# Kernel optimization log

Hardware: AMD Instinct MI355X
Metric: run time of the kernel (lower is better)

Reference implementation:

```python
import jax, jax.numpy as jnp
import numpy as np
from jax import lax

RADIUS = [1, 3, 5, 9, 13, 21]
RATE = 1
K = 4            # shift radius -> (2K+1)^2 = 81 shifts
EPS = 1e-8       # torch.cosine_similarity eps


def setup_inputs() -> dict:
    key = jax.random.key(0)
    k1, k2, k3, k4 = jax.random.split(key, 4)
    b, cin, cout, h, w = 2, 128, 128, 96, 128
    x = jax.random.normal(k1, (b, cout, h, w), dtype=jnp.float32)
    y = jax.random.normal(k2, (b, cin, h, w), dtype=jnp.float32)
    # 6 dilated conv branches, all Conv2d(cin, cout, 3) -> stacked (6, O, I, 3, 3)
    weights = jax.random.normal(k3, (6, cout, cin, 3, 3), dtype=jnp.float32) * 0.05
    biases = jax.random.normal(k4, (6, cout), dtype=jnp.float32) * 0.05
    return {"x": x, "y": y, "weights": weights, "biases": biases}


def _forward(x, y, weights, biases):
    b, c, h, w = y.shape
    k = K
    # reflect-pad y by k, then 'same' dilated convs (zero padding = dilation)
    y_pad = jnp.pad(y, ((0, 0), (0, 0), (k, k), (k, k)), mode="reflect")

    # precompute grouped query features and their norms once
    xg = x.reshape(b, 4, -1, h, w)                      # (b,4,c/4,h,w)
    xn = jnp.sqrt(jnp.sum(xg * xg, axis=2))             # (b,4,h,w)

    # per-branch conv outputs over the padded extent, grouped, with cached norms
    branches = []
    for idx, r in enumerate(RADIUS):
        d = r * RATE
        yo = lax.conv_general_dilated(
            y_pad, weights[idx], window_strides=(1, 1),
            padding=[(d, d), (d, d)], rhs_dilation=(d, d),
            dimension_numbers=("NCHW", "OIHW", "NCHW"),
        ) + biases[idx][None, :, None, None]            # (b,cout,h+2k,w+2k)
        yg = yo.reshape(b, 4, -1, h + 2 * k, w + 2 * k)
        yn = jnp.sqrt(jnp.sum(yg * yg, axis=2))          # (b,4,h+2k,w+2k)
        branches.append((yg, yn))

    result = []
    for i in range(-k, k + 1):
        for j in range(-k, k + 1):
            sx, sy = k + i, k + j
            corrs = []
            for yg, yn in branches:
                ygs = yg[:, :, :, sx:sx + h, sy:sy + w]
                yns = yn[:, :, sx:sx + h, sy:sy + w]
                dot = jnp.einsum("bgchw,bgchw->bghw", xg, ygs)
                corrs.append(dot / jnp.maximum(xn * yns, EPS))
            result.append(jnp.concatenate(corrs, axis=1))  # (b,24,h,w)
    return jnp.stack(result, axis=2)                       # (b,24,81,h,w)


def reference(x, y, weights, biases):
    return _forward(x, y, weights, biases)
```

## Files before the change

kernel.cpp:

```cpp
#include <hip/hip_runtime.h>
#include <math.h>

#define B 2
#define CH 128
#define H 96
#define W 128
#define HP 104
#define WP 136
#define KPAD 4
#define NSHIFT 81
#define NBR 6
#define HW (H*W)
#define HWP (HP*WP)
#define NTILE 111

typedef _Float16 h2 __attribute__((ext_vector_type(2)));
typedef _Float16 half8 __attribute__((ext_vector_type(8)));
typedef float floatx4 __attribute__((ext_vector_type(4)));

__device__ __constant__ int d_radius[NBR] = {1, 3, 5, 9, 13, 21};

__device__ __forceinline__ void async16(const _Float16* g, _Float16* l) {
    __builtin_amdgcn_global_load_lds(
        (const __attribute__((address_space(1))) unsigned int*)g,
        (__attribute__((address_space(3))) unsigned int*)l, 16, 0, 0);
}

__global__ __launch_bounds__(256) void convert_y_kernel(const float* __restrict__ y,
                                                        _Float16* __restrict__ yt16) {
    int gid = blockIdx.x * 256 + threadIdx.x;
    if (gid >= B * HW * CH) return;
    int c = gid & 127;
    int rest = gid >> 7;
    int hw = rest % HW;
    int b = rest / HW;
    yt16[gid] = (_Float16)y[((size_t)(b * CH + c)) * HW + hw];
}

__global__ __launch_bounds__(256) void convert_w_kernel(const float* __restrict__ w,
                                                        _Float16* __restrict__ w16t,
                                                        _Float16* __restrict__ zbuf) {
    int gid = blockIdx.x * 256 + threadIdx.x;
    if (gid < 256) zbuf[gid] = (_Float16)0.0f;
    if (gid >= NBR * 9 * CH * CH) return;
    int ci = gid & 127;
    int co = (gid >> 7) & 127;
    int rest = gid >> 14;
    int tap = rest % 9;
    int br = rest / 9;
    w16t[gid] = (_Float16)w[(((size_t)(br * CH + co)) * CH + ci) * 9 + tap];
}

__global__ __launch_bounds__(256) void convert_x_kernel(const float* __restrict__ x,
                                                        h2* __restrict__ xh) {
    int gid = blockIdx.x * 256 + threadIdx.x;
    if (gid >= B * 4 * 16 * HW) return;
    int pix = gid % HW;
    int rest = gid / HW;
    int p = rest & 15;
    int bgg = rest >> 4;
    int g = bgg & 3, b = bgg >> 2;
    int c0 = g * 32 + 2 * p;
    h2 v;
    v[0] = (_Float16)x[((size_t)(b * CH + c0)) * HW + pix];
    v[1] = (_Float16)x[((size_t)(b * CH + c0 + 1)) * HW + pix];
    xh[gid] = v;
}

__global__ __launch_bounds__(256) void xn_kernel(const float* __restrict__ x,
                                                 float* __restrict__ xn) {
    int idx = blockIdx.x * 256 + threadIdx.x;
    if (idx >= B * 4 * HW) return;
    int pix = idx % HW;
    int bg  = idx / HW;
    int g = bg & 3, b = bg >> 2;
    const float* xp = x + (size_t)(b * CH + g * 32) * HW + pix;
    float s = 0.f;
    #pragma unroll
    for (int c = 0; c < 32; c++) { float v = xp[(size_t)c * HW]; s += v * v; }
    xn[idx] = sqrtf(s);
}

__global__ __launch_bounds__(256) void yn_kernel(const h2* __restrict__ ygh,
                                                 float* __restrict__ yn_all, int total) {
    int idx = blockIdx.x * 256 + threadIdx.x;
    if (idx >= total) return;
    int pix = idx % HWP;
    int rest = idx / HWP;
    const h2* yp = ygh + ((size_t)rest * 16) * HWP + pix;
    float s = 0.f;
    #pragma unroll
    for (int p = 0; p < 16; p++) {
        h2 v = yp[(size_t)p * HWP];
        float a = (float)v[0], c = (float)v[1];
        s += a * a + c * c;
    }
    yn_all[idx] = sqrtf(s);
}

__global__ __launch_bounds__(256) void conv_mfma(const _Float16* __restrict__ yt16,
                                                 const _Float16* __restrict__ w16t,
                                                 const _Float16* __restrict__ zbuf,
                                                 const float* __restrict__ biases,
                                                 h2* __restrict__ ygh) {
    const int tid = threadIdx.x;
    const int lane = tid & 63;
    const int wv = tid >> 6;
    const int tile = blockIdx.x;
    const int br = blockIdx.y;
    const int b = blockIdx.z;
    const int d = d_radius[br];
    const int px0 = tile * 128;

    __shared__ __align__(16) _Float16 Al[128 * 32];
    __shared__ __align__(16) _Float16 Bl[128 * 32];

    const int l16 = tid & 3;
    int ph[2], pw[2];
    bool pval[2];
    #pragma unroll
    for (int s = 0; s < 2; ++s) {
        int pixl = s * 64 + (tid >> 2);
        int pix = px0 + pixl;
        pval[s] = pix < HWP;
        int phh = pix / WP;
        ph[s] = phh; pw[s] = pix - phh * WP;
    }

    const _Float16* ytb = yt16 + (size_t)b * HW * CH;
    const _Float16* wbr = w16t + (size_t)br * 9 * CH * CH;

    floatx4 acc[4][4];
    #pragma unroll
    for (int i = 0; i < 4; i++)
        #pragma unroll
        for (int j = 0; j < 4; j++) {
            floatx4 z = {0.f, 0.f, 0.f, 0.f};
            acc[i][j] = z;
        }

    const int mrow = (wv & 1) * 64 + (lane & 15);
    const int ncol = (wv >> 1) * 64 + (lane & 15);
    const int kq = (lane >> 4) * 8;

    for (int tap = 0; tap < 9; ++tap) {
        const int dkh = (tap / 3 - 1) * d;
        const int dkw = (tap % 3 - 1) * d;
        const _Float16* brow[2];
        #pragma unroll
        for (int s = 0; s < 2; ++s) {
            int gr = ph[s] + dkh, gc = pw[s] + dkw;
            bool v = pval[s] && ((unsigned)gr < (unsigned)HP) && ((unsigned)gc < (unsigned)WP);
            const _Float16* p;
            if (v) {
                int yr = gr - KPAD; yr = yr < 0 ? -yr : (yr >= H ? 2 * (H - 1) - yr : yr);
                int yc = gc - KPAD; yc = yc < 0 ? -yc : (yc >= W ? 2 * (W - 1) - yc : yc);
                p = ytb + ((size_t)(yr * W + yc)) * CH + l16 * 8;
            } else {
                p = zbuf + l16 * 8;
            }
            brow[s] = p;
        }
        const _Float16* wa = wbr + tap * CH * CH + (tid >> 2) * CH + l16 * 8;

        for (int ck = 0; ck < 4; ++ck) {
            const int ci0 = ck * 32;
            async16(wa + ci0,            Al + wv * 512);
            async16(wa + 64 * CH + ci0,  Al + 2048 + wv * 512);
            async16(brow[0] + ci0,       Bl + wv * 512);
            async16(brow[1] + ci0,       Bl + 2048 + wv * 512);
            __syncthreads();

            half8 af[4], bf[4];
            #pragma unroll
            for (int i = 0; i < 4; i++) af[i] = *(const half8*)&Al[(mrow + i * 16) * 32 + kq];
            #pragma unroll
            for (int j = 0; j < 4; j++) bf[j] = *(const half8*)&Bl[(ncol + j * 16) * 32 + kq];
            #pragma unroll
            for (int i = 0; i < 4; i++)
                #pragma unroll
                for (int j = 0; j < 4; j++)
                    acc[i][j] = __builtin_amdgcn_mfma_f32_16x16x32_f16(af[i], bf[j], acc[i][j], 0, 0, 0);
            __syncthreads();
        }
    }

    #pragma unroll
    for (int i = 0; i < 4; i++) {
        int m0 = (wv & 1) * 64 + i * 16 + (lane >> 4) * 4;
        int g0 = (m0 >> 5);
        int pp = (m0 & 31) >> 1;
        float b0 = biases[br * CH + m0];
        float b1 = biases[br * CH + m0 + 1];
        float b2 = biases[br * CH + m0 + 2];
        float b3 = biases[br * CH + m0 + 3];
        h2* outp = ygh + (((size_t)(br * B + b) * 4 + g0) * 16 + pp) * HWP;
        #pragma unroll
        for (int j = 0; j < 4; j++) {
            int pix = px0 + (wv >> 1) * 64 + j * 16 + (lane & 15);
            if (pix < HWP) {
                h2 v0, v1;
                v0[0] = (_Float16)(acc[i][j][0] + b0);
                v0[1] = (_Float16)(acc[i][j][1] + b1);
                v1[0] = (_Float16)(acc[i][j][2] + b2);
                v1[1] = (_Float16)(acc[i][j][3] + b3);
                outp[pix] = v0;
                outp[(size_t)HWP + pix] = v1;
            }
        }
    }
}

#define CPAIR 4
__global__ __launch_bounds__(256) void corr2_kernel(const h2* __restrict__ xh,
                                                    const h2* __restrict__ ygh,
                                                    const float* __restrict__ xn,
                                                    const float* __restrict__ yn_all,
                                                    float* __restrict__ out) {
    const int tid = threadIdx.x;
    const int row = tid >> 5;
    const int col4 = (tid & 31) * 4;
    const int H0 = blockIdx.x * 8;
    const int bg = blockIdx.y;
    const int g = bg & 3, b = bg >> 2;
    const int brl = blockIdx.z;
    const int hh = H0 + row;

    __shared__ __align__(16) _Float16 yt[CPAIR * 340 * 8];

    const h2* ygb = ygh + ((size_t)((brl * B + b) * 4 + g) * 16) * HWP;
    const h2* xb  = xh  + ((size_t)(b * 4 + g) * 16) * HW;
    const float* ynb = yn_all + (size_t)((brl * B + b) * 4 + g) * HWP;

    float xnv[4];
    *(floatx4*)xnv = *(const floatx4*)(xn + (size_t)(b * 4 + g) * HW + hh * W + col4);

    for (int chunk = 0; chunk < 3; ++chunk) {
        const int row0 = H0 + chunk * 3;
        float acc[108];
        #pragma unroll
        for (int s = 0; s < 108; ++s) acc[s] = 0.f;

        for (int p0 = 0; p0 < 16; p0 += CPAIR) {
            __syncthreads();
            for (int i = tid; i < CPAIR * 340; i += 256) {
                int pr = i / 340, off = i - pr * 340;
                const _Float16* src =
                    (const _Float16*)(ygb + (size_t)(p0 + pr) * HWP + row0 * WP) + off * 8;
                async16(src, yt + i * 8);
            }
            __syncthreads();
            #pragma unroll
            for (int cp = 0; cp < CPAIR; ++cp) {
                h2 x2[4];
                *(half8*)x2 = *(const half8*)(xb + (size_t)(p0 + cp) * HW + hh * W + col4);
                #pragma unroll
                for (int sx = 0; sx < 3; ++sx) {
                    h2 yv[12];
                    const _Float16* yr = yt + (cp * 1360 + (row + sx) * 136 + col4) * 2;
                    ((half8*)yv)[0] = *(const half8*)(yr);
                    ((half8*)yv)[1] = *(const half8*)(yr + 8);
                    ((half8*)yv)[2] = *(const half8*)(yr + 16);
                    #pragma unroll
                    for (int sy = 0; sy < 9; ++sy)
                        #pragma unroll
                        for (int j = 0; j < 4; ++j)
                            acc[(sx * 9 + sy) * 4 + j] = __builtin_amdgcn_fdot2(
                                x2[j], yv[sy + j], acc[(sx * 9 + sy) * 4 + j], false);
                }
            }
        }

        #pragma unroll
        for (int sxl = 0; sxl < 3; ++sxl) {
            int sx = chunk * 3 + sxl;
            float ynv[12];
            const float* yp = ynb + (size_t)(hh + sx) * WP + col4;
            *(floatx4*)&ynv[0] = *(const floatx4*)(yp);
            *(floatx4*)&ynv[4] = *(const floatx4*)(yp + 4);
            *(floatx4*)&ynv[8] = *(const floatx4*)(yp + 8);
            float* ob = out + ((size_t)(b * 24 + brl * 4 + g) * NSHIFT + sx * 9) * HW
                        + hh * W + col4;
            #pragma unroll
            for (int sy = 0; sy < 9; ++sy) {
                float o[4];
                #pragma unroll
                for (int j = 0; j < 4; ++j) {
                    float den = xnv[j] * ynv[j + sy];
                    den = den > 1e-8f ? den : 1e-8f;
                    o[j] = acc[(sxl * 9 + sy) * 4 + j] / den;
                }
                *(floatx4*)(ob + (size_t)sy * HW) = *(floatx4*)o;
            }
        }
    }
}

extern "C" void kernel_launch(void* const* d_in, const int* in_sizes, int n_in,
                              void* d_out, int out_size, void* d_ws, size_t ws_size,
                              hipStream_t stream) {
    const float* x       = (const float*)d_in[0];
    const float* y       = (const float*)d_in[1];
    const float* weights = (const float*)d_in[2];
    const float* biases  = (const float*)d_in[3];
    float* out = (float*)d_out;

    const size_t ygh_b = (size_t)NBR * B * 4 * 16 * HWP * 4;
    const size_t yn_b  = (size_t)NBR * B * 4 * HWP * 4;
    const size_t xn_b  = (size_t)B * 4 * HW * 4;
    const size_t yt_b  = (size_t)B * HW * CH * 2;
    const size_t wt_b  = (size_t)NBR * 9 * CH * CH * 2;
    const size_t xh_b  = (size_t)B * 4 * 16 * HW * 4;

    char* p = (char*)d_ws;
    h2* ygh       = (h2*)p;       p += ygh_b;
    float* yn_all = (float*)p;    p += yn_b;
    float* xn     = (float*)p;    p += xn_b;
    _Float16* yt16 = (_Float16*)p; p += yt_b;
    _Float16* w16t = (_Float16*)p; p += wt_b;
    h2* xh        = (h2*)p;       p += xh_b;
    _Float16* zbuf = (_Float16*)p;

    convert_y_kernel<<<(B * HW * CH + 255) / 256, 256, 0, stream>>>(y, yt16);
    convert_w_kernel<<<(NBR * 9 * CH * CH + 255) / 256, 256, 0, stream>>>(weights, w16t, zbuf);
    convert_x_kernel<<<(B * 4 * 16 * HW + 255) / 256, 256, 0, stream>>>(x, xh);
    xn_kernel<<<(B * 4 * HW + 255) / 256, 256, 0, stream>>>(x, xn);

    conv_mfma<<<dim3(NTILE, NBR, B), 256, 0, stream>>>(yt16, w16t, zbuf, biases, ygh);

    int tot = NBR * B * 4 * HWP;
    yn_kernel<<<(tot + 255) / 256, 256, 0, stream>>>(ygh, yn_all, tot);

    corr2_kernel<<<dim3(12, 8, NBR), 256, 0, stream>>>(xh, ygh, xn, yn_all, out);
}
```

Before: 381.6 us.

## Fuse y-norm into conv epilogue, merge x prep, LDS-transpose y conversion

Computes the per-group y norms inside the conv MFMA epilogue from fp32 accumulators with a cross-lane shuffle reduction, removing the separate yn kernel and its re-read of the fp16 conv output. Merges the x fp16 conversion and x-norm kernels into one pass over x. Replaces the strided per-element y transpose with an LDS-tiled transpose that writes 16-byte vectors. The norms now come from fp32 values rather than the rounded fp16 ones, which changes numerics slightly, and the conv epilogue uses more registers.

```diff
diff --git a/kernel.cpp b/kernel.cpp
--- a/kernel.cpp
+++ b/kernel.cpp
@@ -26,15 +26,40 @@
         (__attribute__((address_space(3))) unsigned int*)l, 16, 0, 0);
 }
 
-__global__ __launch_bounds__(256) void convert_y_kernel(const float* __restrict__ y,
-                                                        _Float16* __restrict__ yt16) {
-    int gid = blockIdx.x * 256 + threadIdx.x;
-    if (gid >= B * HW * CH) return;
-    int c = gid & 127;
-    int rest = gid >> 7;
-    int hw = rest % HW;
-    int b = rest / HW;
-    yt16[gid] = (_Float16)y[((size_t)(b * CH + c)) * HW + hw];
+__global__ __launch_bounds__(256) void prep_y(const float* __restrict__ y,
+                                              _Float16* __restrict__ yt16) {
+    __shared__ h2 tile[64 * 129];
+    const int tid = threadIdx.x;
+    const int b = blockIdx.y;
+    const int pix0 = blockIdx.x * 128;
+    const int half = tid >> 7;
+    const int pl = tid & 127;
+
+    const float* yb = y + (size_t)b * CH * HW + pix0 + pl;
+    #pragma unroll
+    for (int k = 0; k < 32; ++k) {
+        int c = half * 64 + 2 * k;
+        float v0 = yb[(size_t)c * HW];
+        float v1 = yb[(size_t)(c + 1) * HW];
+        h2 v; v[0] = (_Float16)v0; v[1] = (_Float16)v1;
+        tile[(half * 32 + k) * 129 + pl] = v;
+    }
+    __syncthreads();
+
+    _Float16* ob = yt16 + ((size_t)b * HW + pix0) * CH;
+    #pragma unroll
+    for (int it = 0; it < 8; ++it) {
+        int pix = it * 16 + (tid >> 4);
+        int c2b = (tid & 15) * 4;
+        h2 t0 = tile[(c2b + 0) * 129 + pix];
+        h2 t1 = tile[(c2b + 1) * 129 + pix];
+        h2 t2 = tile[(c2b + 2) * 129 + pix];
+        h2 t3 = tile[(c2b + 3) * 129 + pix];
+        half8 o;
+        o[0] = t0[0]; o[1] = t0[1]; o[2] = t1[0]; o[3] = t1[1];
+        o[4] = t2[0]; o[5] = t2[1]; o[6] = t3[0]; o[7] = t3[1];
+        *(half8*)(ob + (size_t)pix * CH + (tid & 15) * 8) = o;
+    }
 }
 
 __global__ __launch_bounds__(256) void convert_w_kernel(const float* __restrict__ w,
@@ -51,58 +76,34 @@
     w16t[gid] = (_Float16)w[(((size_t)(br * CH + co)) * CH + ci) * 9 + tap];
 }
 
-__global__ __launch_bounds__(256) void convert_x_kernel(const float* __restrict__ x,
-                                                        h2* __restrict__ xh) {
-    int gid = blockIdx.x * 256 + threadIdx.x;
-    if (gid >= B * 4 * 16 * HW) return;
-    int pix = gid % HW;
-    int rest = gid / HW;
-    int p = rest & 15;
-    int bgg = rest >> 4;
-    int g = bgg & 3, b = bgg >> 2;
-    int c0 = g * 32 + 2 * p;
-    h2 v;
-    v[0] = (_Float16)x[((size_t)(b * CH + c0)) * HW + pix];
-    v[1] = (_Float16)x[((size_t)(b * CH + c0 + 1)) * HW + pix];
-    xh[gid] = v;
-}
-
-__global__ __launch_bounds__(256) void xn_kernel(const float* __restrict__ x,
-                                                 float* __restrict__ xn) {
-    int idx = blockIdx.x * 256 + threadIdx.x;
-    if (idx >= B * 4 * HW) return;
-    int pix = idx % HW;
-    int bg  = idx / HW;
-    int g = bg & 3, b = bg >> 2;
-    const float* xp = x + (size_t)(b * CH + g * 32) * HW + pix;
-    float s = 0.f;
-    #pragma unroll
-    for (int c = 0; c < 32; c++) { float v = xp[(size_t)c * HW]; s += v * v; }
-    xn[idx] = sqrtf(s);
-}
-
-__global__ __launch_bounds__(256) void yn_kernel(const h2* __restrict__ ygh,
-                                                 float* __restrict__ yn_all, int total) {
-    int idx = blockIdx.x * 256 + threadIdx.x;
-    if (idx >= total) return;
-    int pix = idx % HWP;
-    int rest = idx / HWP;
-    const h2* yp = ygh + ((size_t)rest * 16) * HWP + pix;
-    float s = 0.f;
-    #pragma unroll
-    for (int p = 0; p < 16; p++) {
-        h2 v = yp[(size_t)p * HWP];
-        float a = (float)v[0], c = (float)v[1];
-        s += a * a + c * c;
-    }
-    yn_all[idx] = sqrtf(s);
+__global__ __launch_bounds__(256) void prep_x(const float* __restrict__ x,
+                                              h2* __restrict__ xh,
+                                              float* __restrict__ xn) {
+    const int b = blockIdx.y;
+    const int pix = blockIdx.x * 256 + threadIdx.x;
+    const float* xb = x + (size_t)b * CH * HW + pix;
+    #pragma unroll
+    for (int g = 0; g < 4; ++g) {
+        float s = 0.f;
+        #pragma unroll
+        for (int p = 0; p < 16; ++p) {
+            int c = g * 32 + 2 * p;
+            float v0 = xb[(size_t)c * HW];
+            float v1 = xb[(size_t)(c + 1) * HW];
+            h2 v; v[0] = (_Float16)v0; v[1] = (_Float16)v1;
+            xh[((size_t)((b * 4 + g) * 16 + p)) * HW + pix] = v;
+            s += v0 * v0 + v1 * v1;
+        }
+        xn[(size_t)(b * 4 + g) * HW + pix] = sqrtf(s);
+    }
 }
 
 __global__ __launch_bounds__(256) void conv_mfma(const _Float16* __restrict__ yt16,
                                                  const _Float16* __restrict__ w16t,
                                                  const _Float16* __restrict__ zbuf,
                                                  const float* __restrict__ biases,
-                                                 h2* __restrict__ ygh) {
+                                                 h2* __restrict__ ygh,
+                                                 float* __restrict__ yn_all) {
     const int tid = threadIdx.x;
     const int lane = tid & 63;
     const int wv = tid >> 6;
@@ -185,6 +186,12 @@
         }
     }
 
+    float yna[2][4];
+    #pragma unroll
+    for (int gs = 0; gs < 2; ++gs)
+        #pragma unroll
+        for (int j = 0; j < 4; ++j) yna[gs][j] = 0.f;
+
     #pragma unroll
     for (int i = 0; i < 4; i++) {
         int m0 = (wv & 1) * 64 + i * 16 + (lane >> 4) * 4;
@@ -199,13 +206,35 @@
         for (int j = 0; j < 4; j++) {
             int pix = px0 + (wv >> 1) * 64 + j * 16 + (lane & 15);
             if (pix < HWP) {
+                float f0 = acc[i][j][0] + b0;
+                float f1 = acc[i][j][1] + b1;
+                float f2 = acc[i][j][2] + b2;
+                float f3 = acc[i][j][3] + b3;
+                yna[i >> 1][j] += f0 * f0 + f1 * f1 + f2 * f2 + f3 * f3;
                 h2 v0, v1;
-                v0[0] = (_Float16)(acc[i][j][0] + b0);
-                v0[1] = (_Float16)(acc[i][j][1] + b1);
-                v1[0] = (_Float16)(acc[i][j][2] + b2);
-                v1[1] = (_Float16)(acc[i][j][3] + b3);
+                v0[0] = (_Float16)f0;
+                v0[1] = (_Float16)f1;
+                v1[0] = (_Float16)f2;
+                v1[1] = (_Float16)f3;
                 outp[pix] = v0;
                 outp[(size_t)HWP + pix] = v1;
+            }
+        }
+    }
+
+    #pragma unroll
+    for (int gs = 0; gs < 2; ++gs) {
+        #pragma unroll
+        for (int j = 0; j < 4; ++j) {
+            float s = yna[gs][j];
+            s += __shfl_xor(s, 16);
+            s += __shfl_xor(s, 32);
+            if ((lane >> 4) == 0) {
+                int pix = px0 + (wv >> 1) * 64 + j * 16 + lane;
+                if (pix < HWP) {
+                    int g = (wv & 1) * 2 + gs;
+                    yn_all[((size_t)((br * B + b) * 4 + g)) * HWP + pix] = sqrtf(s);
+                }
             }
         }
     }
@@ -321,15 +350,11 @@
     h2* xh        = (h2*)p;       p += xh_b;
     _Float16* zbuf = (_Float16*)p;
 
-    convert_y_kernel<<<(B * HW * CH + 255) / 256, 256, 0, stream>>>(y, yt16);
+    prep_y<<<dim3(HW / 128, B), 256, 0, stream>>>(y, yt16);
     convert_w_kernel<<<(NBR * 9 * CH * CH + 255) / 256, 256, 0, stream>>>(weights, w16t, zbuf);
-    convert_x_kernel<<<(B * 4 * 16 * HW + 255) / 256, 256, 0, stream>>>(x, xh);
-    xn_kernel<<<(B * 4 * HW + 255) / 256, 256, 0, stream>>>(x, xn);
-
-    conv_mfma<<<dim3(NTILE, NBR, B), 256, 0, stream>>>(yt16, w16t, zbuf, biases, ygh);
-
-    int tot = NBR * B * 4 * HWP;
-    yn_kernel<<<(tot + 255) / 256, 256, 0, stream>>>(ygh, yn_all, tot);
+    prep_x<<<dim3(HW / 256, B), 256, 0, stream>>>(x, xh, xn);
+
+    conv_mfma<<<dim3(NTILE, NBR, B), 256, 0, stream>>>(yt16, w16t, zbuf, biases, ygh, yn_all);
 
     corr2_kernel<<<dim3(12, 8, NBR), 256, 0, stream>>>(xh, ygh, xn, yn_all, out);
 }
```

New measurement: 367.8 us. -3.6%, faster.
